# Performance work log

Hardware: AMD Instinct MI355X
Metric: run time of the kernel (lower is better)

## Reference

```python
import jax, jax.numpy as jnp
import numpy as np
import math

B, S, D, DH, R = 2, 2048, 1024, 64, 2


def _hex_grid(radius):
    coords = []
    for q in range(-radius, radius + 1):
        for r in range(max(-radius, -q - radius), min(radius, -q + radius) + 1):
            coords.append((q, r))
    return coords


def _adjacency(coords):
    idx = {c: i for i, c in enumerate(coords)}
    H = len(coords)
    A = np.zeros((H, H), dtype=np.float32)
    dirs = [(1, 0), (1, -1), (0, -1), (-1, 0), (-1, 1), (0, 1)]
    for (q, r), i in idx.items():
        for dq, dr in dirs:
            j = idx.get((q + dq, r + dr))
            if j is not None:
                A[i, j] = 1.0
    return A


def setup_inputs() -> dict:
    key = jax.random.key(0)
    ks = jax.random.split(key, 10)
    coords_list = _hex_grid(R)
    H = len(coords_list)  # 19 heads for radius 2
    coords = jnp.asarray(np.array(coords_list, dtype=np.float32))  # [H,2]
    A = _adjacency(coords_list) + np.eye(H, dtype=np.float32)      # self-loops
    adj_norm = jnp.asarray(A / A.sum(axis=1, keepdims=True))       # row-normalized [H,H]
    sd = 1.0 / math.sqrt(D)
    return {
        "x": jax.random.normal(ks[0], (B, S, D), jnp.float32),
        "coords": coords,
        "w_q": jax.random.normal(ks[1], (H, D, DH), jnp.float32) * sd,
        "w_k": jax.random.normal(ks[2], (H, D, DH), jnp.float32) * sd,
        "w_v": jax.random.normal(ks[3], (H, D, DH), jnp.float32) * sd,
        "wb1": jax.random.normal(ks[4], (2, D), jnp.float32) * 0.5,
        "bb1": jnp.zeros((D,), jnp.float32),
        "wb2": jax.random.normal(ks[5], (D, DH), jnp.float32) * sd,
        "bb2": jnp.zeros((DH,), jnp.float32),
        "w_mix": jax.random.normal(ks[6], (DH, DH), jnp.float32) / math.sqrt(DH),
        "adj_norm": adj_norm,
        "w_o": jax.random.normal(ks[7], (H * DH, D), jnp.float32) * sd,
    }


def reference(x, coords, w_q, w_k, w_v, wb1, bb1, wb2, bb2, w_mix, adj_norm, w_o):
    # coordinate bias: shared MLP mapping hex coord -> d_head bias, added to queries
    bias = jax.nn.relu(coords @ wb1 + bb1) @ wb2 + bb2          # [H,DH]
    # all heads vectorized: q/k/v [B,H,S,DH]
    q = jnp.einsum("bsd,hde->bhse", x, w_q) + bias[None, :, None, :]
    k = jnp.einsum("bsd,hde->bhse", x, w_k)
    v = jnp.einsum("bsd,hde->bhse", x, w_v)
    scores = jnp.einsum("bhse,bhte->bhst", q, k) / math.sqrt(DH)  # [B,H,S,S]
    attn = jax.nn.softmax(scores, axis=-1)
    heads = jnp.einsum("bhst,bhte->bhse", attn, v)               # [B,H,S,DH]
    # GNN mixing over the hex-grid adjacency (residual message passing)
    msg = jax.nn.relu(jnp.einsum("bhse,ef->bhsf", heads, w_mix))
    mixed = heads + jnp.einsum("hg,bgsf->bhsf", adj_norm, msg)   # [B,H,S,DH]
    # concat heads then output projection
    Bx, H, Sx, Dh = mixed.shape
    concat = jnp.transpose(mixed, (0, 2, 1, 3)).reshape(Bx, Sx, H * Dh)
    return concat @ w_o                                          # [B,S,D]
```

## Files before the change

kernel.cpp:

```cpp
#include <hip/hip_runtime.h>
#include <hip/hip_bf16.h>

#define H 19
#define Bv 2
#define Sv 2048
#define Dv 1024
#define DHv 64
#define KK2 (2*H*DHv)
#define QSCALE 0.1803368801111204f

typedef __bf16 bf16x8 __attribute__((ext_vector_type(8)));
typedef float f32x4 __attribute__((ext_vector_type(4)));

__device__ __forceinline__ ushort f2bf(float f) {
    uint u = __float_as_uint(f);
    u = (u + 0x7fffu + ((u >> 16) & 1u)) >> 16;
    return (ushort)u;
}

__device__ __forceinline__ uint cvtpk(float lo, float hi) {
    uint r;
    asm("v_cvt_pk_bf16_f32 %0, %1, %2" : "=v"(r) : "v"(lo), "v"(hi));
    return r;
}

__device__ __forceinline__ float fexp2(float x) {
#if __has_builtin(__builtin_amdgcn_exp2f)
    return __builtin_amdgcn_exp2f(x);
#else
    return exp2f(x);
#endif
}

__device__ __forceinline__ void gll16(const ushort* g, ushort* l) {
    __builtin_amdgcn_global_load_lds(
        (const __attribute__((address_space(1))) unsigned int*)g,
        (__attribute__((address_space(3))) unsigned int*)l, 16, 0, 0);
}

#define PBIAS_AT 0
#define PWO2_AT  (PBIAS_AT + H)
#define PWMIX_AT (PWO2_AT + 304)
#define PWPK_AT  (PWMIX_AT + 1)
#define PX_AT    (PWPK_AT + 912)
#define PREP_N   (PX_AT + 2048)

__global__ __launch_bounds__(256) void prep_all(
    const float* __restrict__ x,  const float* __restrict__ wq,
    const float* __restrict__ wk, const float* __restrict__ wv,
    const float* __restrict__ wo, const float* __restrict__ adj,
    const float* __restrict__ wm, const float* __restrict__ coords,
    const float* __restrict__ wb1, const float* __restrict__ bb1,
    const float* __restrict__ wb2, const float* __restrict__ bb2,
    ushort* __restrict__ xbf, ushort* __restrict__ wpackT,
    ushort* __restrict__ wmixT, ushort* __restrict__ woTcat,
    float* __restrict__ bias)
{
    __shared__ char psm[18432];
    const int bid = blockIdx.x;
    const int tid = threadIdx.x;

    if (bid < PWO2_AT) {
        float* part = (float*)psm;
        int hh = bid - PBIAS_AT;
        int e = tid & 63, quar = tid >> 6;
        float c0 = coords[hh*2], c1 = coords[hh*2+1];
        float acc = (quar == 0) ? bb2[e] : 0.f;
        int d0 = quar*256;
        for (int d = d0; d < d0+256; ++d) {
            float t2 = fmaxf(c0*wb1[d] + c1*wb1[Dv+d] + bb1[d], 0.f);
            acc += t2 * wb2[d*DHv + e];
        }
        if (quar) part[(quar-1)*64 + e] = acc;
        __syncthreads();
        if (quar == 0) bias[hh*DHv + e] = acc + part[e] + part[64+e] + part[128+e];
    } else if (bid < PWMIX_AT) {
        int j2 = bid - PWO2_AT;
        int nt = j2 & 15, g = j2 >> 4;
        int e = tid >> 2, n4 = tid & 3;
        float acc[16], part1[16];
        #pragma unroll
        for (int j = 0; j < 16; ++j) { acc[j] = 0.f; part1[j] = 0.f; }
        for (int h2 = 0; h2 < H; ++h2) {
            float a = adj[h2*H + g];
            const float* rp = wo + (size_t)(h2*64 + e)*Dv + nt*64 + n4*16;
            #pragma unroll
            for (int j4 = 0; j4 < 4; ++j4) {
                float4 v = *(const float4*)&rp[j4*4];
                acc[j4*4+0] += a*v.x; acc[j4*4+1] += a*v.y;
                acc[j4*4+2] += a*v.z; acc[j4*4+3] += a*v.w;
                if (h2 == g) {
                    part1[j4*4+0] = v.x; part1[j4*4+1] = v.y;
                    part1[j4*4+2] = v.z; part1[j4*4+3] = v.w;
                }
            }
        }
        ushort* T = (ushort*)psm;
        #pragma unroll
        for (int j = 0; j < 16; ++j) {
            int nl = n4*16 + j;
            T[nl*72 + e]         = f2bf(part1[j]);
            T[64*72 + nl*72 + e] = f2bf(acc[j]);
        }
        __syncthreads();
        int nl = tid >> 2, c = tid & 3;
        {
            ushort* dst = &woTcat[(size_t)(nt*64 + nl)*KK2 + g*64 + c*16];
            uint4 v0 = *(uint4*)&T[nl*72 + c*16];
            uint4 v1 = *(uint4*)&T[nl*72 + c*16 + 8];
            *(uint4*)dst = v0; *(uint4*)(dst + 8) = v1;
        }
        {
            ushort* dst = &woTcat[(size_t)(nt*64 + nl)*KK2 + H*DHv + g*64 + c*16];
            uint4 v0 = *(uint4*)&T[64*72 + nl*72 + c*16];
            uint4 v1 = *(uint4*)&T[64*72 + nl*72 + c*16 + 8];
            *(uint4*)dst = v0; *(uint4*)(dst + 8) = v1;
        }
    } else if (bid == PWMIX_AT) {
        int e = tid >> 2, f4 = tid & 3;
        #pragma unroll
        for (int j = 0; j < 16; ++j) {
            int f = f4*16 + j;
            wmixT[e*64 + f] = f2bf(wm[f*64 + e]);
        }
    } else if (bid < PX_AT) {
        ushort* T = (ushort*)psm;
        int i = bid - PWPK_AT;
        int dt = i & 15, t = (i >> 4) % 3, h = (i >> 4) / 3;
        const float* w = (t == 0) ? wq : (t == 1) ? wk : wv;
        w += (size_t)h*Dv*DHv;
        int row = tid >> 2, c4 = tid & 3;
        #pragma unroll
        for (int q4 = 0; q4 < 4; ++q4) {
            float4 v = *(const float4*)&w[(size_t)(dt*64+row)*DHv + c4*16 + q4*4];
            T[(c4*16 + q4*4 + 0)*65 + row] = f2bf(v.x);
            T[(c4*16 + q4*4 + 1)*65 + row] = f2bf(v.y);
            T[(c4*16 + q4*4 + 2)*65 + row] = f2bf(v.z);
            T[(c4*16 + q4*4 + 3)*65 + row] = f2bf(v.w);
        }
        __syncthreads();
        #pragma unroll
        for (int i2 = 0; i2 < 2; ++i2) {
            int f = tid + i2*256;
            int e = f >> 3, c = f & 7;
            uint u[4];
            #pragma unroll
            for (int j = 0; j < 4; ++j) {
                uint lo = T[e*65 + c*8 + 2*j];
                uint hi = T[e*65 + c*8 + 2*j + 1];
                u[j] = lo | (hi << 16);
            }
            *(uint4*)&wpackT[((size_t)h*192 + t*64 + e)*Dv + dt*64 + c*8] = make_uint4(u[0],u[1],u[2],u[3]);
        }
    } else {
        int idx = ((bid - PX_AT)*256 + tid)*8;
        float4 a = *(const float4*)&x[idx];
        float4 b = *(const float4*)&x[idx+4];
        uint4 o;
        o.x = cvtpk(a.x, a.y); o.y = cvtpk(a.z, a.w);
        o.z = cvtpk(b.x, b.y); o.w = cvtpk(b.z, b.w);
        *(uint4*)&xbf[idx] = o;
    }
}

__global__ __launch_bounds__(256) void qkv_mfma(const ushort* __restrict__ xbf,
                                                const ushort* __restrict__ wpackT,
                                                const float* __restrict__ bias,
                                                ushort* __restrict__ qbf,
                                                ushort* __restrict__ kbf,
                                                ushort* __restrict__ vtbf) {
    const int mt = blockIdx.x, h = blockIdx.y;
    const int m0 = mt*64;
    const int tid = threadIdx.x;
    const int w = tid >> 6, lane = tid & 63;
    const int g = lane >> 4, r = lane & 15;

    __shared__ char lds[8192 + 24576];
    char* Xs = lds;
    char* Ws = lds + 8192;
    ushort* VtL = (ushort*)lds;

    f32x4 acc[4][3];
    const f32x4 zf = {0.f,0.f,0.f,0.f};
    #pragma unroll
    for (int m = 0; m < 4; ++m)
        #pragma unroll
        for (int n = 0; n < 3; ++n) acc[m][n] = zf;

    const ushort* xb = xbf + (size_t)m0*Dv;
    const ushort* wb = wpackT + (size_t)h*192*Dv;

    for (int kt = 0; kt < Dv; kt += 64) {
        __syncthreads();
        #pragma unroll
        for (int i = 0; i < 2; ++i) {
            int f = tid + i*256;
            int row = f >> 3, c = f & 7;
            *(bf16x8*)(Xs + row*128 + ((c*16) ^ ((row & 7) << 4))) =
                *(const bf16x8*)(xb + (size_t)row*Dv + kt + c*8);
        }
        #pragma unroll
        for (int i = 0; i < 6; ++i) {
            int f = tid + i*256;
            int row = f >> 3, c = f & 7;
            *(bf16x8*)(Ws + row*128 + ((c*16) ^ ((row & 7) << 4))) =
                *(const bf16x8*)(wb + (size_t)row*Dv + kt + c*8);
        }
        __syncthreads();
        #pragma unroll
        for (int kk = 0; kk < 2; ++kk) {
            bf16x8 a[4], bfr[3];
            #pragma unroll
            for (int m = 0; m < 4; ++m) {
                int row = m*16 + r;
                a[m] = *(const bf16x8*)(Xs + row*128 + (((kk*32 + g*8)*2) ^ ((row & 7) << 4)));
            }
            #pragma unroll
            for (int n = 0; n < 3; ++n) {
                int row = (w*3 + n)*16 + r;
                bfr[n] = *(const bf16x8*)(Ws + row*128 + (((kk*32 + g*8)*2) ^ ((row & 7) << 4)));
            }
            #pragma unroll
            for (int m = 0; m < 4; ++m)
                #pragma unroll
                for (int n = 0; n < 3; ++n)
                    acc[m][n] = __builtin_amdgcn_mfma_f32_16x16x32_bf16(a[m], bfr[n], acc[m][n], 0, 0, 0);
        }
    }

    __syncthreads();

    const int bb = m0 >> 11;
    const int s0 = m0 & 2047;
    #pragma unroll
    for (int m = 0; m < 4; ++m) {
        #pragma unroll
        for (int n = 0; n < 3; ++n) {
            int ng = w*3 + n;
            int t = ng >> 2;
            int e = (ng & 3)*16 + r;
            if (t == 0) {
                float bvv = bias[h*DHv + e];
                #pragma unroll
                for (int reg = 0; reg < 4; ++reg) {
                    int ss = s0 + m*16 + g*4 + reg;
                    qbf[(((size_t)bb*H + h)*Sv + ss)*DHv + e] = f2bf((acc[m][n][reg] + bvv)*QSCALE);
                }
            } else if (t == 1) {
                #pragma unroll
                for (int reg = 0; reg < 4; ++reg) {
                    int ss = s0 + m*16 + g*4 + reg;
                    kbf[(((size_t)bb*H + h)*Sv + ss)*DHv + e] = f2bf(acc[m][n][reg]);
                }
            } else {
                #pragma unroll
                for (int reg = 0; reg < 4; ++reg) {
                    int sl = m*16 + g*4 + reg;
                    VtL[e*66 + sl] = f2bf(acc[m][n][reg]);
                }
            }
        }
    }
    __syncthreads();
    #pragma unroll
    for (int i = 0; i < 2; ++i) {
        int f = tid + i*256;
        int dh = f >> 3, sc = f & 7;
        uint u[4];
        #pragma unroll
        for (int j = 0; j < 4; ++j) {
            uint lo = VtL[dh*66 + sc*8 + 2*j];
            uint hi = VtL[dh*66 + sc*8 + 2*j + 1];
            u[j] = lo | (hi << 16);
        }
        *(uint4*)&vtbf[(((size_t)bb*H + h)*DHv + dh)*Sv + s0 + sc*8] = make_uint4(u[0],u[1],u[2],u[3]);
    }
}

__global__ __launch_bounds__(256) void attn_mfma(const ushort* __restrict__ qg,
                                                 const ushort* __restrict__ kg,
                                                 const ushort* __restrict__ vtg,
                                                 const ushort* __restrict__ wmixT,
                                                 ushort* __restrict__ headsbf,
                                                 ushort* __restrict__ msgbf) {
    const int hw = blockIdx.x;
    const int logical = (hw & 7) * 152 + (hw >> 3);
    const int qt = logical & 31;
    const int hb = logical >> 5;
    const int h = hb % H, b = hb / H;

    const int tid = threadIdx.x;
    const int w = tid >> 6, lane = tid & 63;
    const int g = lane >> 4, r = lane & 15;
    const int srow = lane >> 3, scl = lane & 7;

    __shared__ ushort Ks[4096];
    __shared__ ushort Vs[4096];
    __shared__ ushort Ps[4][1024];

    const size_t bh = (size_t)b*H + h;
    const ushort* kb = kg + bh*Sv*DHv;
    const ushort* vb = vtg + bh*DHv*Sv;
    const ushort* qb = qg + (bh*Sv + qt*64 + w*16 + r)*DHv;

    bf16x8 qf0 = *(const bf16x8*)(qb + g*8);
    bf16x8 qf1 = *(const bf16x8*)(qb + 32 + g*8);

    float m_run = -1e30f, l_run = 0.f;
    f32x4 o[4];
    const f32x4 zf = {0.f,0.f,0.f,0.f};
    o[0]=zf; o[1]=zf; o[2]=zf; o[3]=zf;

    for (int jt = 0; jt < Sv/64; ++jt) {
        __syncthreads();
        #pragma unroll
        for (int is = 0; is < 2; ++is) {
            int row = w*16 + is*8 + srow;
            int kcol = (scl ^ (row & 7)) * 8;
            gll16(kb + (size_t)(jt*64 + row)*DHv + kcol, &Ks[(w*16 + is*8)*64]);
            gll16(vb + (size_t)row*Sv + jt*64 + kcol, &Vs[(w*16 + is*8)*64]);
        }
        asm volatile("s_waitcnt vmcnt(0)" ::: "memory");
        __syncthreads();

        f32x4 sc[4];
        sc[0]=zf; sc[1]=zf; sc[2]=zf; sc[3]=zf;
        #pragma unroll
        for (int kk = 0; kk < 2; ++kk) {
            bf16x8 qf = kk ? qf1 : qf0;
            #pragma unroll
            for (int nt = 0; nt < 4; ++nt) {
                int kvrow = nt*16 + r;
                bf16x8 kf = *(const bf16x8*)((const char*)Ks + kvrow*128 +
                                             ((kk*64 + g*16) ^ ((kvrow & 7) << 4)));
                sc[nt] = __builtin_amdgcn_mfma_f32_16x16x32_bf16(kf, qf, sc[nt], 0, 0, 0);
            }
        }

        float pmax = sc[0][0];
        #pragma unroll
        for (int nt = 0; nt < 4; ++nt)
            #pragma unroll
            for (int reg = 0; reg < 4; ++reg)
                pmax = fmaxf(pmax, sc[nt][reg]);
        pmax = fmaxf(pmax, __shfl_xor(pmax, 16));
        pmax = fmaxf(pmax, __shfl_xor(pmax, 32));

        if (__any(pmax > m_run + 8.0f)) {
            float mn = fmaxf(m_run, pmax);
            float corr = fexp2(m_run - mn);
            l_run *= corr;
            #pragma unroll
            for (int nt2 = 0; nt2 < 4; ++nt2) {
                o[nt2][0] *= corr; o[nt2][1] *= corr;
                o[nt2][2] *= corr; o[nt2][3] *= corr;
            }
            m_run = mn;
        }

        float lsum = 0.f;
        #pragma unroll
        for (int nt = 0; nt < 4; ++nt) {
            #pragma unroll
            for (int reg = 0; reg < 4; ++reg) {
                float p = fexp2(sc[nt][reg] - m_run);
                sc[nt][reg] = p;
                lsum += p;
            }
        }
        lsum += __shfl_xor(lsum, 16);
        lsum += __shfl_xor(lsum, 32);
        l_run += lsum;

        ushort* pw = Ps[w];
        #pragma unroll
        for (int nt = 0; nt < 4; ++nt) {
            uint u0 = cvtpk(sc[nt][0], sc[nt][1]);
            uint u1 = cvtpk(sc[nt][2], sc[nt][3]);
            int chunk = (2*nt + (g >> 1)) ^ (r & 7);
            *(uint2*)((char*)pw + r*128 + (chunk << 4) + ((g & 1)*8)) = make_uint2(u0, u1);
        }

        #pragma unroll
        for (int kk = 0; kk < 2; ++kk) {
            bf16x8 pa = *(const bf16x8*)((const char*)pw + r*128 +
                                         (((kk*4 + g) ^ (r & 7)) << 4));
            #pragma unroll
            for (int nt2 = 0; nt2 < 4; ++nt2) {
                int dh = nt2*16 + r;
                bf16x8 vf = *(const bf16x8*)((const char*)Vs + dh*128 +
                                             ((kk*64 + g*16) ^ ((dh & 7) << 4)));
                o[nt2] = __builtin_amdgcn_mfma_f32_16x16x32_bf16(vf, pa, o[nt2], 0, 0, 0);
            }
        }
    }

    float inv = 1.0f / l_run;
    ushort* hp = headsbf + (bh*Sv + qt*64 + w*16 + r)*DHv;
    ushort* pw = Ps[w];
    #pragma unroll
    for (int nt2 = 0; nt2 < 4; ++nt2) {
        uint u0 = cvtpk(o[nt2][0]*inv, o[nt2][1]*inv);
        uint u1 = cvtpk(o[nt2][2]*inv, o[nt2][3]*inv);
        *(uint2*)(hp + nt2*16 + g*4) = make_uint2(u0, u1);
        int chunk = (2*nt2 + (g >> 1)) ^ (r & 7);
        *(uint2*)((char*)pw + r*128 + (chunk << 4) + ((g & 1)*8)) = make_uint2(u0, u1);
    }

    bf16x8 wmf[2][4];
    #pragma unroll
    for (int kk = 0; kk < 2; ++kk)
        #pragma unroll
        for (int nt = 0; nt < 4; ++nt)
            wmf[kk][nt] = *(const bf16x8*)(wmixT + (nt*16 + r)*64 + kk*32 + g*8);

    f32x4 macc[4];
    macc[0]=zf; macc[1]=zf; macc[2]=zf; macc[3]=zf;
    #pragma unroll
    for (int kk = 0; kk < 2; ++kk) {
        bf16x8 pa = *(const bf16x8*)((const char*)pw + r*128 +
                                     (((kk*4 + g) ^ (r & 7)) << 4));
        #pragma unroll
        for (int nt = 0; nt < 4; ++nt)
            macc[nt] = __builtin_amdgcn_mfma_f32_16x16x32_bf16(wmf[kk][nt], pa, macc[nt], 0, 0, 0);
    }
    ushort* mp = msgbf + (bh*Sv + qt*64 + w*16 + r)*DHv;
    #pragma unroll
    for (int nt = 0; nt < 4; ++nt) {
        uint u0 = cvtpk(fmaxf(macc[nt][0], 0.f), fmaxf(macc[nt][1], 0.f));
        uint u1 = cvtpk(fmaxf(macc[nt][2], 0.f), fmaxf(macc[nt][3], 0.f));
        *(uint2*)(mp + nt*16 + g*4) = make_uint2(u0, u1);
    }
}

__global__ __launch_bounds__(256) void out_mfma(const ushort* __restrict__ headsbf,
                                                const ushort* __restrict__ msgbf,
                                                const ushort* __restrict__ woTcat,
                                                float* __restrict__ out) {
    const int mt = blockIdx.x, nt2 = blockIdx.y;
    const int m0 = mt*64, n0 = nt2*128;
    const int tid = threadIdx.x;
    const int w = tid >> 6, lane = tid & 63;
    const int g = lane >> 4, r = lane & 15;

    __shared__ char lds[8192 + 16384];
    char* As = lds;
    char* Bs = lds + 8192;

    const int b = m0 >> 11;
    const int s0 = m0 & 2047;

    f32x4 acc[8];
    const f32x4 zf = {0.f,0.f,0.f,0.f};
    #pragma unroll
    for (int n = 0; n < 8; ++n) acc[n] = zf;

    for (int ktile = 0; ktile < KK2/64; ++ktile) {
        const int hh = (ktile < H) ? ktile : ktile - H;
        const ushort* asrc = ((ktile < H) ? headsbf : msgbf) +
                             ((size_t)((size_t)b*H + hh)*Sv + s0)*DHv;
        __syncthreads();
        #pragma unroll
        for (int i = 0; i < 2; ++i) {
            int f = tid + i*256;
            int row = f >> 3, c = f & 7;
            *(bf16x8*)(As + row*128 + ((c*16) ^ ((row & 7) << 4))) =
                *(const bf16x8*)(asrc + (size_t)row*DHv + c*8);
        }
        #pragma unroll
        for (int i = 0; i < 4; ++i) {
            int f = tid + i*256;
            int row = f >> 3, c = f & 7;
            *(bf16x8*)(Bs + row*128 + ((c*16) ^ ((row & 7) << 4))) =
                *(const bf16x8*)(woTcat + (size_t)(n0 + row)*KK2 + ktile*64 + c*8);
        }
        __syncthreads();
        #pragma unroll
        for (int kk = 0; kk < 2; ++kk) {
            int arow = w*16 + r;
            bf16x8 a = *(const bf16x8*)(As + arow*128 + (((kk*32 + g*8)*2) ^ ((arow & 7) << 4)));
            #pragma unroll
            for (int n = 0; n < 8; ++n) {
                int brow = n*16 + r;
                bf16x8 bfr = *(const bf16x8*)(Bs + brow*128 + (((kk*32 + g*8)*2) ^ ((brow & 7) << 4)));
                acc[n] = __builtin_amdgcn_mfma_f32_16x16x32_bf16(a, bfr, acc[n], 0, 0, 0);
            }
        }
    }

    #pragma unroll
    for (int n = 0; n < 8; ++n) {
        #pragma unroll
        for (int reg = 0; reg < 4; ++reg) {
            int grow = m0 + w*16 + g*4 + reg;
            out[(size_t)grow*Dv + n0 + n*16 + r] = acc[n][reg];
        }
    }
}

extern "C" void kernel_launch(void* const* d_in, const int* in_sizes, int n_in,
                              void* d_out, int out_size, void* d_ws, size_t ws_size,
                              hipStream_t stream) {
    const float* x      = (const float*)d_in[0];
    const float* coords = (const float*)d_in[1];
    const float* w_q    = (const float*)d_in[2];
    const float* w_k    = (const float*)d_in[3];
    const float* w_v    = (const float*)d_in[4];
    const float* wb1    = (const float*)d_in[5];
    const float* bb1    = (const float*)d_in[6];
    const float* wb2    = (const float*)d_in[7];
    const float* bb2    = (const float*)d_in[8];
    const float* w_mix  = (const float*)d_in[9];
    const float* adj    = (const float*)d_in[10];
    const float* w_o    = (const float*)d_in[11];

    char* ws = (char*)d_ws;
    const size_t QKV_BYTES = (size_t)Bv*H*Sv*DHv*2;
    const size_t XBF_BYTES = (size_t)Bv*Sv*Dv*2;
    const size_t WPK_BYTES = (size_t)H*192*Dv*2;

    size_t off = 0;
    float*  bias  = (float*)(ws + off);  off += 16384;
    ushort* qbf   = (ushort*)(ws + off); off += QKV_BYTES;
    ushort* kbf   = (ushort*)(ws + off); off += QKV_BYTES;
    ushort* vtbf  = (ushort*)(ws + off); off += QKV_BYTES;
    ushort* hdbf  = (ushort*)(ws + off); off += QKV_BYTES;
    ushort* xbf   = (ushort*)(ws + off);
    ushort* msgbf = xbf;
    off += XBF_BYTES;
    ushort* wpkT  = (ushort*)(ws + off); off += WPK_BYTES;
    ushort* wmixT = (ushort*)(ws + off); off += 8192;
    ushort* woTc  = (ushort*)(ws + off); off += (size_t)Dv*KK2*2;
    float*  out   = (float*)d_out;

    prep_all<<<PREP_N, 256, 0, stream>>>(x, w_q, w_k, w_v, w_o, adj, w_mix,
                                         coords, wb1, bb1, wb2, bb2,
                                         xbf, wpkT, wmixT, woTc, bias);
    qkv_mfma<<<dim3(64, H), 256, 0, stream>>>(xbf, wpkT, bias, qbf, kbf, vtbf);
    attn_mfma<<<1216, 256, 0, stream>>>(qbf, kbf, vtbf, wmixT, hdbf, msgbf);
    out_mfma<<<dim3(64, 8), 256, 0, stream>>>(hdbf, msgbf, woTc, out);
}
```

Measured before the change: 345.4 us.

## Process two query groups per wave in attention and split bias MLP kernel

The attention kernel now runs 2 waves per block, each handling 32 query rows as two 16-row groups. K and V fragments are loaded from LDS once and reused across both groups, halving LDS fragment reads per MFMA. The coordinate-bias MLP moves out of the prep kernel into its own 4x19-block kernel that writes partial sums, which qkv_mfma adds together. In exchange attention uses more registers per wave and has fewer waves per block to hide latency, and the bias work costs an extra kernel launch.

```diff
diff --git a/kernel.cpp b/kernel.cpp
--- a/kernel.cpp
+++ b/kernel.cpp
@@ -38,43 +38,25 @@
         (__attribute__((address_space(3))) unsigned int*)l, 16, 0, 0);
 }
 
-#define PBIAS_AT 0
-#define PWO2_AT  (PBIAS_AT + H)
-#define PWMIX_AT (PWO2_AT + 304)
-#define PWPK_AT  (PWMIX_AT + 1)
-#define PX_AT    (PWPK_AT + 912)
+#define PWO2_AT  0
+#define PWPK_AT  (PWO2_AT + 304)
+#define PWMIX_AT (PWPK_AT + 912)
+#define PX_AT    (PWMIX_AT + 1)
 #define PREP_N   (PX_AT + 2048)
 
-__global__ __launch_bounds__(256) void prep_all(
+__global__ __launch_bounds__(256) void prep_misc(
     const float* __restrict__ x,  const float* __restrict__ wq,
     const float* __restrict__ wk, const float* __restrict__ wv,
     const float* __restrict__ wo, const float* __restrict__ adj,
-    const float* __restrict__ wm, const float* __restrict__ coords,
-    const float* __restrict__ wb1, const float* __restrict__ bb1,
-    const float* __restrict__ wb2, const float* __restrict__ bb2,
+    const float* __restrict__ wm,
     ushort* __restrict__ xbf, ushort* __restrict__ wpackT,
-    ushort* __restrict__ wmixT, ushort* __restrict__ woTcat,
-    float* __restrict__ bias)
+    ushort* __restrict__ wmixT, ushort* __restrict__ woTcat)
 {
     __shared__ char psm[18432];
     const int bid = blockIdx.x;
     const int tid = threadIdx.x;
 
-    if (bid < PWO2_AT) {
-        float* part = (float*)psm;
-        int hh = bid - PBIAS_AT;
-        int e = tid & 63, quar = tid >> 6;
-        float c0 = coords[hh*2], c1 = coords[hh*2+1];
-        float acc = (quar == 0) ? bb2[e] : 0.f;
-        int d0 = quar*256;
-        for (int d = d0; d < d0+256; ++d) {
-            float t2 = fmaxf(c0*wb1[d] + c1*wb1[Dv+d] + bb1[d], 0.f);
-            acc += t2 * wb2[d*DHv + e];
-        }
-        if (quar) part[(quar-1)*64 + e] = acc;
-        __syncthreads();
-        if (quar == 0) bias[hh*DHv + e] = acc + part[e] + part[64+e] + part[128+e];
-    } else if (bid < PWMIX_AT) {
+    if (bid < PWPK_AT) {
         int j2 = bid - PWO2_AT;
         int nt = j2 & 15, g = j2 >> 4;
         int e = tid >> 2, n4 = tid & 3;
@@ -116,14 +98,7 @@
             uint4 v1 = *(uint4*)&T[64*72 + nl*72 + c*16 + 8];
             *(uint4*)dst = v0; *(uint4*)(dst + 8) = v1;
         }
-    } else if (bid == PWMIX_AT) {
-        int e = tid >> 2, f4 = tid & 3;
-        #pragma unroll
-        for (int j = 0; j < 16; ++j) {
-            int f = f4*16 + j;
-            wmixT[e*64 + f] = f2bf(wm[f*64 + e]);
-        }
-    } else if (bid < PX_AT) {
+    } else if (bid < PWMIX_AT) {
         ushort* T = (ushort*)psm;
         int i = bid - PWPK_AT;
         int dt = i & 15, t = (i >> 4) % 3, h = (i >> 4) / 3;
@@ -151,6 +126,13 @@
                 u[j] = lo | (hi << 16);
             }
             *(uint4*)&wpackT[((size_t)h*192 + t*64 + e)*Dv + dt*64 + c*8] = make_uint4(u[0],u[1],u[2],u[3]);
+        }
+    } else if (bid == PWMIX_AT) {
+        int e = tid >> 2, f4 = tid & 3;
+        #pragma unroll
+        for (int j = 0; j < 16; ++j) {
+            int f = f4*16 + j;
+            wmixT[e*64 + f] = f2bf(wm[f*64 + e]);
         }
     } else {
         int idx = ((bid - PX_AT)*256 + tid)*8;
@@ -163,9 +145,31 @@
     }
 }
 
+__global__ __launch_bounds__(256) void bias_part_kernel(
+    const float* __restrict__ coords, const float* __restrict__ wb1,
+    const float* __restrict__ bb1, const float* __restrict__ wb2,
+    const float* __restrict__ bb2, float* __restrict__ bias_part) {
+    const int bq = blockIdx.x, hh = blockIdx.y;
+    const int e = threadIdx.x & 63, sub = threadIdx.x >> 6;
+    __shared__ float part[3][64];
+    float c0 = coords[hh*2], c1 = coords[hh*2+1];
+    float acc = (bq == 0 && sub == 0) ? bb2[e] : 0.f;
+    const int d0 = bq*256 + sub*64;
+    #pragma unroll 8
+    for (int i = 0; i < 64; ++i) {
+        int d = d0 + i;
+        float t2 = fmaxf(c0*wb1[d] + c1*wb1[Dv+d] + bb1[d], 0.f);
+        acc += t2 * wb2[d*DHv + e];
+    }
+    if (sub) part[sub-1][e] = acc;
+    __syncthreads();
+    if (sub == 0)
+        bias_part[(bq*H + hh)*DHv + e] = acc + part[0][e] + part[1][e] + part[2][e];
+}
+
 __global__ __launch_bounds__(256) void qkv_mfma(const ushort* __restrict__ xbf,
                                                 const ushort* __restrict__ wpackT,
-                                                const float* __restrict__ bias,
+                                                const float* __restrict__ bias_part,
                                                 ushort* __restrict__ qbf,
                                                 ushort* __restrict__ kbf,
                                                 ushort* __restrict__ vtbf) {
@@ -240,7 +244,8 @@
             int t = ng >> 2;
             int e = (ng & 3)*16 + r;
             if (t == 0) {
-                float bvv = bias[h*DHv + e];
+                float bvv = bias_part[(0*H + h)*DHv + e] + bias_part[(1*H + h)*DHv + e]
+                          + bias_part[(2*H + h)*DHv + e] + bias_part[(3*H + h)*DHv + e];
                 #pragma unroll
                 for (int reg = 0; reg < 4; ++reg) {
                     int ss = s0 + m*16 + g*4 + reg;
@@ -277,7 +282,7 @@
     }
 }
 
-__global__ __launch_bounds__(256) void attn_mfma(const ushort* __restrict__ qg,
+__global__ __launch_bounds__(128) void attn_mfma(const ushort* __restrict__ qg,
                                                  const ushort* __restrict__ kg,
                                                  const ushort* __restrict__ vtg,
                                                  const ushort* __restrict__ wmixT,
@@ -296,140 +301,169 @@
 
     __shared__ ushort Ks[4096];
     __shared__ ushort Vs[4096];
-    __shared__ ushort Ps[4][1024];
+    __shared__ ushort Ps[2][1024];
 
     const size_t bh = (size_t)b*H + h;
     const ushort* kb = kg + bh*Sv*DHv;
     const ushort* vb = vtg + bh*DHv*Sv;
-    const ushort* qb = qg + (bh*Sv + qt*64 + w*16 + r)*DHv;
-
-    bf16x8 qf0 = *(const bf16x8*)(qb + g*8);
-    bf16x8 qf1 = *(const bf16x8*)(qb + 32 + g*8);
-
-    float m_run = -1e30f, l_run = 0.f;
-    f32x4 o[4];
+
+    bf16x8 qf[2][2];
+    #pragma unroll
+    for (int grp = 0; grp < 2; ++grp) {
+        const ushort* qb = qg + (bh*Sv + qt*64 + w*32 + grp*16 + r)*DHv;
+        qf[grp][0] = *(const bf16x8*)(qb + g*8);
+        qf[grp][1] = *(const bf16x8*)(qb + 32 + g*8);
+    }
+
+    float m_run[2] = {-1e30f, -1e30f}, l_run[2] = {0.f, 0.f};
+    f32x4 o[2][4];
     const f32x4 zf = {0.f,0.f,0.f,0.f};
-    o[0]=zf; o[1]=zf; o[2]=zf; o[3]=zf;
+    #pragma unroll
+    for (int grp = 0; grp < 2; ++grp)
+        #pragma unroll
+        for (int n = 0; n < 4; ++n) o[grp][n] = zf;
 
     for (int jt = 0; jt < Sv/64; ++jt) {
         __syncthreads();
         #pragma unroll
-        for (int is = 0; is < 2; ++is) {
-            int row = w*16 + is*8 + srow;
-            int kcol = (scl ^ (row & 7)) * 8;
-            gll16(kb + (size_t)(jt*64 + row)*DHv + kcol, &Ks[(w*16 + is*8)*64]);
-            gll16(vb + (size_t)row*Sv + jt*64 + kcol, &Vs[(w*16 + is*8)*64]);
+        for (int is = 0; is < 4; ++is) {
+            int row = w*32 + is*8 + srow;
+            int kcol = (scl ^ srow) * 8;
+            gll16(kb + (size_t)(jt*64 + row)*DHv + kcol, &Ks[(w*32 + is*8)*64]);
+            gll16(vb + (size_t)row*Sv + jt*64 + kcol, &Vs[(w*32 + is*8)*64]);
         }
         asm volatile("s_waitcnt vmcnt(0)" ::: "memory");
         __syncthreads();
 
-        f32x4 sc[4];
-        sc[0]=zf; sc[1]=zf; sc[2]=zf; sc[3]=zf;
-        #pragma unroll
-        for (int kk = 0; kk < 2; ++kk) {
-            bf16x8 qf = kk ? qf1 : qf0;
+        bf16x8 fr[2][4];
+        #pragma unroll
+        for (int kk = 0; kk < 2; ++kk)
             #pragma unroll
             for (int nt = 0; nt < 4; ++nt) {
                 int kvrow = nt*16 + r;
-                bf16x8 kf = *(const bf16x8*)((const char*)Ks + kvrow*128 +
-                                             ((kk*64 + g*16) ^ ((kvrow & 7) << 4)));
-                sc[nt] = __builtin_amdgcn_mfma_f32_16x16x32_bf16(kf, qf, sc[nt], 0, 0, 0);
-            }
-        }
-
-        float pmax = sc[0][0];
+                fr[kk][nt] = *(const bf16x8*)((const char*)Ks + kvrow*128 +
+                                              ((kk*64 + g*16) ^ ((kvrow & 7) << 4)));
+            }
+
+        f32x4 sc[2][4];
+        #pragma unroll
+        for (int grp = 0; grp < 2; ++grp) {
+            sc[grp][0]=zf; sc[grp][1]=zf; sc[grp][2]=zf; sc[grp][3]=zf;
+            #pragma unroll
+            for (int kk = 0; kk < 2; ++kk)
+                #pragma unroll
+                for (int nt = 0; nt < 4; ++nt)
+                    sc[grp][nt] = __builtin_amdgcn_mfma_f32_16x16x32_bf16(
+                        fr[kk][nt], qf[grp][kk], sc[grp][nt], 0, 0, 0);
+        }
+
+        #pragma unroll
+        for (int grp = 0; grp < 2; ++grp) {
+            float pmax = sc[grp][0][0];
+            #pragma unroll
+            for (int nt = 0; nt < 4; ++nt)
+                #pragma unroll
+                for (int reg = 0; reg < 4; ++reg)
+                    pmax = fmaxf(pmax, sc[grp][nt][reg]);
+            pmax = fmaxf(pmax, __shfl_xor(pmax, 16));
+            pmax = fmaxf(pmax, __shfl_xor(pmax, 32));
+
+            if (__any(pmax > m_run[grp] + 8.0f)) {
+                float mn = fmaxf(m_run[grp], pmax);
+                float corr = fexp2(m_run[grp] - mn);
+                l_run[grp] *= corr;
+                #pragma unroll
+                for (int nt2 = 0; nt2 < 4; ++nt2) {
+                    o[grp][nt2][0] *= corr; o[grp][nt2][1] *= corr;
+                    o[grp][nt2][2] *= corr; o[grp][nt2][3] *= corr;
+                }
+                m_run[grp] = mn;
+            }
+
+            float lsum = 0.f;
+            #pragma unroll
+            for (int nt = 0; nt < 4; ++nt) {
+                #pragma unroll
+                for (int reg = 0; reg < 4; ++reg) {
+                    float p = fexp2(sc[grp][nt][reg] - m_run[grp]);
+                    sc[grp][nt][reg] = p;
+                    lsum += p;
+                }
+            }
+            lsum += __shfl_xor(lsum, 16);
+            lsum += __shfl_xor(lsum, 32);
+            l_run[grp] += lsum;
+        }
+
+        #pragma unroll
+        for (int kk = 0; kk < 2; ++kk)
+            #pragma unroll
+            for (int nt2 = 0; nt2 < 4; ++nt2) {
+                int dh = nt2*16 + r;
+                fr[kk][nt2] = *(const bf16x8*)((const char*)Vs + dh*128 +
+                                               ((kk*64 + g*16) ^ ((dh & 7) << 4)));
+            }
+
+        ushort* pw = Ps[w];
+        #pragma unroll
+        for (int grp = 0; grp < 2; ++grp) {
+            #pragma unroll
+            for (int nt = 0; nt < 4; ++nt) {
+                uint u0 = cvtpk(sc[grp][nt][0], sc[grp][nt][1]);
+                uint u1 = cvtpk(sc[grp][nt][2], sc[grp][nt][3]);
+                int chunk = (2*nt + (g >> 1)) ^ (r & 7);
+                *(uint2*)((char*)pw + r*128 + (chunk << 4) + ((g & 1)*8)) = make_uint2(u0, u1);
+            }
+            #pragma unroll
+            for (int kk = 0; kk < 2; ++kk) {
+                bf16x8 pa = *(const bf16x8*)((const char*)pw + r*128 +
+                                             (((kk*4 + g) ^ (r & 7)) << 4));
+                #pragma unroll
+                for (int nt2 = 0; nt2 < 4; ++nt2)
+                    o[grp][nt2] = __builtin_amdgcn_mfma_f32_16x16x32_bf16(
+                        fr[kk][nt2], pa, o[grp][nt2], 0, 0, 0);
+            }
+        }
+    }
+
+    bf16x8 wmf[2][4];
+    #pragma unroll
+    for (int kk = 0; kk < 2; ++kk)
         #pragma unroll
         for (int nt = 0; nt < 4; ++nt)
-            #pragma unroll
-            for (int reg = 0; reg < 4; ++reg)
-                pmax = fmaxf(pmax, sc[nt][reg]);
-        pmax = fmaxf(pmax, __shfl_xor(pmax, 16));
-        pmax = fmaxf(pmax, __shfl_xor(pmax, 32));
-
-        if (__any(pmax > m_run + 8.0f)) {
-            float mn = fmaxf(m_run, pmax);
-            float corr = fexp2(m_run - mn);
-            l_run *= corr;
-            #pragma unroll
-            for (int nt2 = 0; nt2 < 4; ++nt2) {
-                o[nt2][0] *= corr; o[nt2][1] *= corr;
-                o[nt2][2] *= corr; o[nt2][3] *= corr;
-            }
-            m_run = mn;
-        }
-
-        float lsum = 0.f;
-        #pragma unroll
-        for (int nt = 0; nt < 4; ++nt) {
-            #pragma unroll
-            for (int reg = 0; reg < 4; ++reg) {
-                float p = fexp2(sc[nt][reg] - m_run);
-                sc[nt][reg] = p;
-                lsum += p;
-            }
-        }
-        lsum += __shfl_xor(lsum, 16);
-        lsum += __shfl_xor(lsum, 32);
-        l_run += lsum;
-
-        ushort* pw = Ps[w];
-        #pragma unroll
-        for (int nt = 0; nt < 4; ++nt) {
-            uint u0 = cvtpk(sc[nt][0], sc[nt][1]);
-            uint u1 = cvtpk(sc[nt][2], sc[nt][3]);
-            int chunk = (2*nt + (g >> 1)) ^ (r & 7);
+            wmf[kk][nt] = *(const bf16x8*)(wmixT + (nt*16 + r)*64 + kk*32 + g*8);
+
+    ushort* pw = Ps[w];
+    #pragma unroll
+    for (int grp = 0; grp < 2; ++grp) {
+        float inv = 1.0f / l_run[grp];
+        ushort* hp = headsbf + (bh*Sv + qt*64 + w*32 + grp*16 + r)*DHv;
+        #pragma unroll
+        for (int nt2 = 0; nt2 < 4; ++nt2) {
+            uint u0 = cvtpk(o[grp][nt2][0]*inv, o[grp][nt2][1]*inv);
+            uint u1 = cvtpk(o[grp][nt2][2]*inv, o[grp][nt2][3]*inv);
+            *(uint2*)(hp + nt2*16 + g*4) = make_uint2(u0, u1);
+            int chunk = (2*nt2 + (g >> 1)) ^ (r & 7);
             *(uint2*)((char*)pw + r*128 + (chunk << 4) + ((g & 1)*8)) = make_uint2(u0, u1);
         }
-
+        f32x4 macc[4];
+        const f32x4 zf2 = {0.f,0.f,0.f,0.f};
+        macc[0]=zf2; macc[1]=zf2; macc[2]=zf2; macc[3]=zf2;
         #pragma unroll
         for (int kk = 0; kk < 2; ++kk) {
             bf16x8 pa = *(const bf16x8*)((const char*)pw + r*128 +
                                          (((kk*4 + g) ^ (r & 7)) << 4));
             #pragma unroll
-            for (int nt2 = 0; nt2 < 4; ++nt2) {
-                int dh = nt2*16 + r;
-                bf16x8 vf = *(const bf16x8*)((const char*)Vs + dh*128 +
-                                             ((kk*64 + g*16) ^ ((dh & 7) << 4)));
-                o[nt2] = __builtin_amdgcn_mfma_f32_16x16x32_bf16(vf, pa, o[nt2], 0, 0, 0);
-            }
-        }
-    }
-
-    float inv = 1.0f / l_run;
-    ushort* hp = headsbf + (bh*Sv + qt*64 + w*16 + r)*DHv;
-    ushort* pw = Ps[w];
-    #pragma unroll
-    for (int nt2 = 0; nt2 < 4; ++nt2) {
-        uint u0 = cvtpk(o[nt2][0]*inv, o[nt2][1]*inv);
-        uint u1 = cvtpk(o[nt2][2]*inv, o[nt2][3]*inv);
-        *(uint2*)(hp + nt2*16 + g*4) = make_uint2(u0, u1);
-        int chunk = (2*nt2 + (g >> 1)) ^ (r & 7);
-        *(uint2*)((char*)pw + r*128 + (chunk << 4) + ((g & 1)*8)) = make_uint2(u0, u1);
-    }
-
-    bf16x8 wmf[2][4];
-    #pragma unroll
-    for (int kk = 0; kk < 2; ++kk)
-        #pragma unroll
-        for (int nt = 0; nt < 4; ++nt)
-            wmf[kk][nt] = *(const bf16x8*)(wmixT + (nt*16 + r)*64 + kk*32 + g*8);
-
-    f32x4 macc[4];
-    macc[0]=zf; macc[1]=zf; macc[2]=zf; macc[3]=zf;
-    #pragma unroll
-    for (int kk = 0; kk < 2; ++kk) {
-        bf16x8 pa = *(const bf16x8*)((const char*)pw + r*128 +
-                                     (((kk*4 + g) ^ (r & 7)) << 4));
-        #pragma unroll
-        for (int nt = 0; nt < 4; ++nt)
-            macc[nt] = __builtin_amdgcn_mfma_f32_16x16x32_bf16(wmf[kk][nt], pa, macc[nt], 0, 0, 0);
-    }
-    ushort* mp = msgbf + (bh*Sv + qt*64 + w*16 + r)*DHv;
-    #pragma unroll
-    for (int nt = 0; nt < 4; ++nt) {
-        uint u0 = cvtpk(fmaxf(macc[nt][0], 0.f), fmaxf(macc[nt][1], 0.f));
-        uint u1 = cvtpk(fmaxf(macc[nt][2], 0.f), fmaxf(macc[nt][3], 0.f));
-        *(uint2*)(mp + nt*16 + g*4) = make_uint2(u0, u1);
+            for (int nt = 0; nt < 4; ++nt)
+                macc[nt] = __builtin_amdgcn_mfma_f32_16x16x32_bf16(wmf[kk][nt], pa, macc[nt], 0, 0, 0);
+        }
+        ushort* mp = msgbf + (bh*Sv + qt*64 + w*32 + grp*16 + r)*DHv;
+        #pragma unroll
+        for (int nt = 0; nt < 4; ++nt) {
+            uint u0 = cvtpk(fmaxf(macc[nt][0], 0.f), fmaxf(macc[nt][1], 0.f));
+            uint u1 = cvtpk(fmaxf(macc[nt][2], 0.f), fmaxf(macc[nt][3], 0.f));
+            *(uint2*)(mp + nt*16 + g*4) = make_uint2(u0, u1);
+        }
     }
 }
 
@@ -520,7 +554,7 @@
     const size_t WPK_BYTES = (size_t)H*192*Dv*2;
 
     size_t off = 0;
-    float*  bias  = (float*)(ws + off);  off += 16384;
+    float*  biasp = (float*)(ws + off);  off += 32768;
     ushort* qbf   = (ushort*)(ws + off); off += QKV_BYTES;
     ushort* kbf   = (ushort*)(ws + off); off += QKV_BYTES;
     ushort* vtbf  = (ushort*)(ws + off); off += QKV_BYTES;
@@ -533,10 +567,10 @@
     ushort* woTc  = (ushort*)(ws + off); off += (size_t)Dv*KK2*2;
     float*  out   = (float*)d_out;
 
-    prep_all<<<PREP_N, 256, 0, stream>>>(x, w_q, w_k, w_v, w_o, adj, w_mix,
-                                         coords, wb1, bb1, wb2, bb2,
-                                         xbf, wpkT, wmixT, woTc, bias);
-    qkv_mfma<<<dim3(64, H), 256, 0, stream>>>(xbf, wpkT, bias, qbf, kbf, vtbf);
-    attn_mfma<<<1216, 256, 0, stream>>>(qbf, kbf, vtbf, wmixT, hdbf, msgbf);
+    prep_misc<<<PREP_N, 256, 0, stream>>>(x, w_q, w_k, w_v, w_o, adj, w_mix,
+                                          xbf, wpkT, wmixT, woTc);
+    bias_part_kernel<<<dim3(4, H), 256, 0, stream>>>(coords, wb1, bb1, wb2, bb2, biasp);
+    qkv_mfma<<<dim3(64, H), 256, 0, stream>>>(xbf, wpkT, biasp, qbf, kbf, vtbf);
+    attn_mfma<<<1216, 128, 0, stream>>>(qbf, kbf, vtbf, wmixT, hdbf, msgbf);
     out_mfma<<<dim3(64, 8), 256, 0, stream>>>(hdbf, msgbf, woTc, out);
 }
```

Measured after the change: 315.6 us. -8.6%, faster.
